# Optimization experiments

Measured on AMD Instinct MI355X. Metric: run time of the kernel, lower is better.

The kernel has to match this reference:

```python
import jax, jax.numpy as jnp
import numpy as np
import math

N_NODES = 100000
N_EDGES = 1600000
IN_CH = 128
EDGE_DIM = 8
HEADS = 4
C1, C2 = 10, 5  # per-head out channels of conv1/conv2
N_GRAPHS = 64


def setup_inputs() -> dict:
    key = jax.random.key(0)
    k = jax.random.split(key, 26)
    s = 0.05
    d1, d2 = HEADS * C1, HEADS * C2  # 40, 20
    lin = lambda kk, fi, fo: jax.random.normal(kk, (fi, fo), jnp.float32) * s
    inp = {}
    inp['x'] = jax.random.normal(k[0], (N_NODES, IN_CH), jnp.float32)
    inp['edge_index'] = jax.random.randint(k[1], (2, N_EDGES), 0, N_NODES)
    inp['edge_attr'] = jax.random.normal(k[2], (N_EDGES, EDGE_DIM), jnp.float32)
    inp['batch'] = jnp.sort(jax.random.randint(k[3], (N_NODES,), 0, N_GRAPHS))
    # conv1 params (TransformerConv: lin_query/key/value + lin_edge(no bias) + lin_skip)
    inp['Wq1'] = lin(k[4], IN_CH, d1); inp['bq1'] = jnp.zeros((d1,), jnp.float32)
    inp['Wk1'] = lin(k[5], IN_CH, d1); inp['bk1'] = jnp.zeros((d1,), jnp.float32)
    inp['Wv1'] = lin(k[6], IN_CH, d1); inp['bv1'] = jnp.zeros((d1,), jnp.float32)
    inp['We1'] = lin(k[7], EDGE_DIM, d1)
    inp['Ws1'] = lin(k[8], IN_CH, d1); inp['bs1'] = jnp.zeros((d1,), jnp.float32)
    # conv2 params
    inp['Wq2'] = lin(k[9], d1, d2); inp['bq2'] = jnp.zeros((d2,), jnp.float32)
    inp['Wk2'] = lin(k[10], d1, d2); inp['bk2'] = jnp.zeros((d2,), jnp.float32)
    inp['Wv2'] = lin(k[11], d1, d2); inp['bv2'] = jnp.zeros((d2,), jnp.float32)
    inp['We2'] = lin(k[12], EDGE_DIM, d2)
    inp['Ws2'] = lin(k[13], d1, d2); inp['bs2'] = jnp.zeros((d2,), jnp.float32)
    # MLP head
    inp['W1'] = lin(k[14], d2, 10); inp['b1'] = jnp.zeros((10,), jnp.float32)
    inp['W2'] = lin(k[15], 10, 3); inp['b2'] = jnp.zeros((3,), jnp.float32)
    return inp


def _segment_softmax(alpha, dst, n):
    # numerically stable softmax over incoming edges of each target node
    amax = jax.ops.segment_max(alpha, dst, num_segments=n)
    ex = jnp.exp(alpha - amax[dst])
    den = jax.ops.segment_sum(ex, dst, num_segments=n)
    return ex / (den[dst] + 1e-16)


def _transformer_conv(x, src, dst, eattr, Wq, bq, Wk, bk, Wv, bv, We, Ws, bs, heads, ch):
    n = x.shape[0]
    q = (x @ Wq + bq).reshape(n, heads, ch)
    k = (x @ Wk + bk).reshape(n, heads, ch)
    v = (x @ Wv + bv).reshape(n, heads, ch)
    e = (eattr @ We).reshape(-1, heads, ch)          # [E,H,C]
    kj = k[src] + e                                   # gather + edge bias
    alpha = jnp.einsum('ehc,ehc->eh', q[dst], kj) / math.sqrt(ch)
    alpha = _segment_softmax(alpha, dst, n)           # [E,H]
    msg = (v[src] + e) * alpha[:, :, None]
    out = jax.ops.segment_sum(msg, dst, num_segments=n).reshape(n, heads * ch)
    return out + x @ Ws + bs                          # root/skip connection (beta=False)


def reference(x, edge_index, edge_attr, batch, Wq1, bq1, Wk1, bk1, Wv1, bv1, We1, Ws1, bs1, Wq2, bq2, Wk2, bk2, Wv2, bv2, We2, Ws2, bs2, W1, b1, W2, b2):
    src, dst = edge_index[0], edge_index[1]
    h = jax.nn.relu(_transformer_conv(x, src, dst, edge_attr, Wq1, bq1, Wk1, bk1, Wv1, bv1, We1, Ws1, bs1, HEADS, C1))
    h = jax.nn.relu(_transformer_conv(h, src, dst, edge_attr, Wq2, bq2, Wk2, bk2, Wv2, bv2, We2, Ws2, bs2, HEADS, C2))
    # global_mean_pool
    sums = jax.ops.segment_sum(h, batch, num_segments=N_GRAPHS)
    cnt = jax.ops.segment_sum(jnp.ones((h.shape[0],), h.dtype), batch, num_segments=N_GRAPHS)
    pooled = sums / jnp.maximum(cnt, 1.0)[:, None]
    h = jax.nn.relu(pooled @ W1 + b1)
    return h @ W2 + b2
```

## Files before the change

kernel.cpp:

```cpp
#include <hip/hip_runtime.h>
#include <math.h>

__device__ __forceinline__ unsigned bfr_(float f) {
    unsigned u = __float_as_uint(f);
    return (u + 0x7fffu + ((u >> 16) & 1u)) >> 16;
}
__device__ __forceinline__ unsigned pack2_(float lo, float hi) {
    return bfr_(lo) | (bfr_(hi) << 16);
}
__device__ __forceinline__ float unlo_(unsigned u) { return __uint_as_float(u << 16); }
__device__ __forceinline__ float unhi_(unsigned u) { return __uint_as_float(u & 0xffff0000u); }
__device__ __forceinline__ float bf2f_(unsigned short us) {
    return __uint_as_float((unsigned)us << 16);
}

__global__ void k_hist(const int* __restrict__ dst, int* __restrict__ deg, int E) {
    int e = blockIdx.x * 256 + threadIdx.x;
    if (e < E) atomicAdd(&deg[dst[e]], 1);
}

__global__ void k_scan1(const int* __restrict__ deg, int* __restrict__ rp,
                        int* __restrict__ bsum, int n) {
    __shared__ int sh[256];
    int t = threadIdx.x;
    int base = blockIdx.x * 1024 + t * 4;
    int v0 = (base + 0 < n) ? deg[base + 0] : 0;
    int v1 = (base + 1 < n) ? deg[base + 1] : 0;
    int v2 = (base + 2 < n) ? deg[base + 2] : 0;
    int v3 = (base + 3 < n) ? deg[base + 3] : 0;
    int ts = v0 + v1 + v2 + v3;
    sh[t] = ts;
    __syncthreads();
    for (int off = 1; off < 256; off <<= 1) {
        int x = (t >= off) ? sh[t - off] : 0;
        __syncthreads();
        sh[t] += x;
        __syncthreads();
    }
    int run = sh[t] - ts;
    if (base + 0 < n) rp[base + 0] = run;
    run += v0;
    if (base + 1 < n) rp[base + 1] = run;
    run += v1;
    if (base + 2 < n) rp[base + 2] = run;
    run += v2;
    if (base + 3 < n) rp[base + 3] = run;
    if (t == 255) bsum[blockIdx.x] = sh[255];
}

__global__ void k_scan2(int* __restrict__ bsum, int nb) {
    __shared__ int sh[256];
    int t = threadIdx.x;
    int v = (t < nb) ? bsum[t] : 0;
    sh[t] = v;
    __syncthreads();
    for (int off = 1; off < 256; off <<= 1) {
        int x = (t >= off) ? sh[t - off] : 0;
        __syncthreads();
        sh[t] += x;
        __syncthreads();
    }
    if (t < nb) bsum[t] = sh[t] - v;
}

__global__ void k_scan3(int* __restrict__ rp, const int* __restrict__ bsum,
                        int* __restrict__ cur, int n, int total) {
    int t = threadIdx.x;
    int base = blockIdx.x * 1024 + t * 4;
    int add = bsum[blockIdx.x];
    if (base + 0 < n) { rp[base + 0] += add; cur[base + 0] = 0; }
    if (base + 1 < n) { rp[base + 1] += add; cur[base + 1] = 0; }
    if (base + 2 < n) { rp[base + 2] += add; cur[base + 2] = 0; }
    if (base + 3 < n) { rp[base + 3] += add; cur[base + 3] = 0; }
    if (blockIdx.x == 0 && t == 0) rp[n] = total;
}

__global__ void k_scatter(const int* __restrict__ src, const int* __restrict__ dst,
                          const int* __restrict__ rp, int* __restrict__ cur,
                          const float4* __restrict__ ea,
                          unsigned long long* __restrict__ se_perm,
                          uint4* __restrict__ eab, int E) {
    int e = blockIdx.x * 256 + threadIdx.x;
    if (e >= E) return;
    float4 a = ea[(size_t)e * 2 + 0];
    float4 b = ea[(size_t)e * 2 + 1];
    uint4 u;
    u.x = pack2_(a.x, a.y);
    u.y = pack2_(a.z, a.w);
    u.z = pack2_(b.x, b.y);
    u.w = pack2_(b.z, b.w);
    eab[e] = u;
    int d = dst[e];
    int pos = rp[d] + atomicAdd(&cur[d], 1);
    unsigned long long rec =
        ((unsigned long long)(unsigned)e << 32) | (unsigned)src[e];
    __builtin_nontemporal_store(rec, &se_perm[pos]);
}

template <int FIN, int CH, int KTILE, int NPT, int CHPAD>
__global__ __launch_bounds__(256) void k_proj(
    const float* __restrict__ X,
    const float* __restrict__ Wq, const float* __restrict__ Wk,
    const float* __restrict__ Wv, const float* __restrict__ Ws,
    const float* __restrict__ bq, const float* __restrict__ bk,
    const float* __restrict__ bv, const float* __restrict__ bs,
    float* __restrict__ qO, unsigned* __restrict__ kvO,
    unsigned short* __restrict__ sO, int N) {
    constexpr int FOUT = 4 * CH;
    constexpr int STRIDE = 4 * CHPAD;
    constexpr int NPB = 64;
    constexpr int COLS = 4 * FOUT;
    constexpr int NCG = COLS / 10;
    constexpr int NG = 256 / NCG;
    static_assert(NG * NPT == NPB, "geometry");
    constexpr int F4 = FIN / 4;
    __shared__ float xs[FIN * NPB];
    __shared__ float wbuf[KTILE * COLS];
    int t = threadIdx.x;
    int nb = blockIdx.x * NPB;
    for (int i = t; i < NPB * F4; i += 256) {
        int nl = i & 63;
        int k4 = (i >> 6) * 4;
        int node = nb + nl;
        float4 val = make_float4(0.f, 0.f, 0.f, 0.f);
        if (node < N) val = *(const float4*)(X + (size_t)node * FIN + k4);
        xs[(k4 + 0) * NPB + nl] = val.x;
        xs[(k4 + 1) * NPB + nl] = val.y;
        xs[(k4 + 2) * NPB + nl] = val.z;
        xs[(k4 + 3) * NPB + nl] = val.w;
    }
    int cg = t % NCG, ng = t / NCG;
    int which = (cg * 10) / FOUT, cc0 = (cg * 10) % FOUT;
    float acc[NPT][10];
#pragma unroll
    for (int i = 0; i < NPT; ++i)
#pragma unroll
        for (int j = 0; j < 10; ++j) acc[i][j] = 0.f;

    for (int kt = 0; kt < FIN; kt += KTILE) {
        __syncthreads();
        for (int i = t; i < KTILE * (COLS / 4); i += 256) {
            int kk = i / (COLS / 4);
            int c4 = (i % (COLS / 4)) * 4;
            int wh = c4 / FOUT, cc = c4 % FOUT;
            const float* Wsrc = wh == 0 ? Wq : wh == 1 ? Wk : wh == 2 ? Wv : Ws;
            float4 wv = *(const float4*)(Wsrc + (size_t)(kt + kk) * FOUT + cc);
            wbuf[kk * COLS + c4 + 0] = wv.x;
            wbuf[kk * COLS + c4 + 1] = wv.y;
            wbuf[kk * COLS + c4 + 2] = wv.z;
            wbuf[kk * COLS + c4 + 3] = wv.w;
        }
        __syncthreads();
#pragma unroll 4
        for (int kk = 0; kk < KTILE; ++kk) {
            float xv[NPT];
            if constexpr (NPT == 4) {
                float4 x4 = *(const float4*)(xs + (kt + kk) * NPB + ng * 4);
                xv[0] = x4.x; xv[1] = x4.y; xv[2] = x4.z; xv[3] = x4.w;
            } else {
                float2 x2 = *(const float2*)(xs + (kt + kk) * NPB + ng * 2);
                xv[0] = x2.x; xv[1] = x2.y;
            }
            const float2* wp = (const float2*)(wbuf + kk * COLS + cg * 10);
            float wv[10];
#pragma unroll
            for (int jj = 0; jj < 5; ++jj) {
                float2 w2 = wp[jj];
                wv[2 * jj] = w2.x;
                wv[2 * jj + 1] = w2.y;
            }
#pragma unroll
            for (int i = 0; i < NPT; ++i)
#pragma unroll
                for (int j = 0; j < 10; ++j) acc[i][j] += xv[i] * wv[j];
        }
    }
    const float* B = which == 0 ? bq : which == 1 ? bk : which == 2 ? bv : bs;
    float bias[10];
#pragma unroll
    for (int j = 0; j < 10; ++j) bias[j] = B[cc0 + j];
    __syncthreads();
    if (which == 0) {
#pragma unroll
        for (int i = 0; i < NPT; ++i) {
            int node = nb + ng * NPT + i;
            if (node < N)
#pragma unroll
                for (int j = 0; j < 10; ++j) {
                    int col = cc0 + j, hh = col / CH, cc = col % CH;
                    qO[(size_t)node * STRIDE + hh * CHPAD + cc] = acc[i][j] + bias[j];
                }
        }
    } else if (which == 3) {
#pragma unroll
        for (int i = 0; i < NPT; ++i) {
            int node = nb + ng * NPT + i;
            if (node < N)
#pragma unroll
                for (int j = 0; j < 10; ++j)
                    sO[(size_t)node * FOUT + cc0 + j] =
                        (unsigned short)bfr_(acc[i][j] + bias[j]);
        }
    } else if (which == 1) {
#pragma unroll
        for (int i = 0; i < NPT; ++i) {
            int nl = ng * NPT + i;
#pragma unroll
            for (int j = 0; j < 10; ++j) wbuf[nl * FOUT + cc0 + j] = acc[i][j] + bias[j];
        }
    }
    __syncthreads();
    if (which == 2) {
#pragma unroll
        for (int i = 0; i < NPT; ++i) {
            int nl = ng * NPT + i;
            int node = nb + nl;
            if (node < N)
#pragma unroll
                for (int j = 0; j < 10; ++j) {
                    int col = cc0 + j, hh = col / CH, cc = col % CH;
                    float kf = wbuf[nl * FOUT + cc0 + j];
                    kvO[(size_t)node * STRIDE + hh * CHPAD + cc] =
                        pack2_(kf, acc[i][j] + bias[j]);
                }
        }
    }
}

template <int CH, int CHPAD, bool SHIFT>
__global__ __launch_bounds__(256) void k_conv(
    const int* __restrict__ rp, const unsigned long long* __restrict__ se_perm,
    const uint4* __restrict__ eab, const float* __restrict__ We,
    const float* __restrict__ q, const unsigned* __restrict__ kv,
    const unsigned short* __restrict__ skp, float* __restrict__ hout,
    float inv_sqrt, int N) {
    constexpr int D = 4 * CH;
    constexpr int STRIDE = 4 * CHPAD;
    constexpr int RAWN = SHIFT ? CHPAD + 2 : CHPAD;
    constexpr int NLD = RAWN / 4;
    __shared__ float we_s[8 * D];
    for (int i = threadIdx.x; i < 8 * D; i += 256) we_s[i] = We[i];
    __syncthreads();
    int g = blockIdx.x * 256 + threadIdx.x;
    int node = g >> 4;
    int h = g & 3;
    int qtr = (g >> 2) & 3;
    if (node >= N) return;
    int start_off = SHIFT ? ((h * CH) & ~3) : h * CHPAD;
    int rs = rp[node], re = rp[node + 1];
    float qh[CH];
    {
        float qraw[RAWN];
        const float4* qp = (const float4*)(q + (size_t)node * STRIDE + start_off);
#pragma unroll
        for (int i = 0; i < NLD; ++i) *(float4*)&qraw[4 * i] = qp[i];
        if constexpr (SHIFT) {
            if (h & 1) {
#pragma unroll
                for (int c = 0; c < CH; ++c) qraw[c] = qraw[c + 2];
            }
        }
#pragma unroll
        for (int c = 0; c < CH; ++c) qh[c] = qraw[c];
    }
    float qe[8];
#pragma unroll
    for (int j = 0; j < 8; ++j) {
        float sE = 0.f;
#pragma unroll
        for (int c = 0; c < CH; ++c) sE += qh[c] * we_s[j * D + h * CH + c];
        qe[j] = sE;
    }
    float m = -3.0e38f, l = 0.f;
    float accv[CH] = {};
    float acce[8] = {};
    for (int p = rs + qtr; p < re; p += 4) {
        unsigned long long se = se_perm[p];
        int sidx = (int)(unsigned)(se & 0xffffffffu);
        int eid = (int)(unsigned)(se >> 32);
        uint4 eu = eab[eid];
        float ea8[8];
        ea8[0] = unlo_(eu.x); ea8[1] = unhi_(eu.x);
        ea8[2] = unlo_(eu.y); ea8[3] = unhi_(eu.y);
        ea8[4] = unlo_(eu.z); ea8[5] = unhi_(eu.z);
        ea8[6] = unlo_(eu.w); ea8[7] = unhi_(eu.w);
        unsigned kraw[RAWN];
        const uint4* kp = (const uint4*)(kv + (size_t)sidx * STRIDE + start_off);
#pragma unroll
        for (int i = 0; i < NLD; ++i) *(uint4*)&kraw[4 * i] = kp[i];
        if constexpr (SHIFT) {
            if (h & 1) {
#pragma unroll
                for (int c = 0; c < CH; ++c) kraw[c] = kraw[c + 2];
            }
        }
        float a = 0.f;
        float vj[CH];
#pragma unroll
        for (int c = 0; c < CH; ++c) {
            unsigned u = kraw[c];
            a += qh[c] * unlo_(u);
            vj[c] = unhi_(u);
        }
#pragma unroll
        for (int j = 0; j < 8; ++j) a += qe[j] * ea8[j];
        a *= inv_sqrt;
        float mn = fmaxf(m, a);
        float so = __expf(m - mn);
        float w = __expf(a - mn);
        l = l * so + w;
#pragma unroll
        for (int c = 0; c < CH; ++c) accv[c] = accv[c] * so + w * vj[c];
#pragma unroll
        for (int j = 0; j < 8; ++j) acce[j] = acce[j] * so + w * ea8[j];
        m = mn;
    }
#pragma unroll
    for (int mask = 4; mask <= 8; mask <<= 1) {
        float mo = __shfl_xor(m, mask);
        float lo = __shfl_xor(l, mask);
        float mn = fmaxf(m, mo);
        float s1 = (m > -1e37f) ? __expf(m - mn) : 0.f;
        float s2 = (mo > -1e37f) ? __expf(mo - mn) : 0.f;
        l = l * s1 + lo * s2;
#pragma unroll
        for (int c = 0; c < CH; ++c) {
            float ao = __shfl_xor(accv[c], mask);
            accv[c] = accv[c] * s1 + ao * s2;
        }
#pragma unroll
        for (int j = 0; j < 8; ++j) {
            float ao = __shfl_xor(acce[j], mask);
            acce[j] = acce[j] * s1 + ao * s2;
        }
        m = mn;
    }
    if (qtr == 0) {
        float inv = 1.0f / (l + 1e-16f);
#pragma unroll
        for (int c = 0; c < CH; ++c) {
            float ec = 0.f;
#pragma unroll
            for (int j = 0; j < 8; ++j) ec += acce[j] * we_s[j * D + h * CH + c];
            float o = (accv[c] + ec) * inv + bf2f_(skp[(size_t)node * D + h * CH + c]);
            hout[(size_t)node * D + h * CH + c] = fmaxf(o, 0.f);
        }
    }
}

__global__ void k_pool(const float* __restrict__ h2, const int* __restrict__ batch,
                       float* __restrict__ pooled, float* __restrict__ cnt, int N) {
    int t = blockIdx.x * 256 + threadIdx.x;
    int start = t * 16;
    if (start >= N) return;
    int end = min(start + 16, N);
    float acc[20];
#pragma unroll
    for (int c = 0; c < 20; ++c) acc[c] = 0.f;
    int cg = batch[start];
    float run = 0.f;
    for (int n = start; n < end; ++n) {
        int g = batch[n];
        if (g != cg) {
#pragma unroll
            for (int c = 0; c < 20; ++c) atomicAdd(&pooled[cg * 20 + c], acc[c]);
            atomicAdd(&cnt[cg], run);
#pragma unroll
            for (int c = 0; c < 20; ++c) acc[c] = 0.f;
            run = 0.f;
            cg = g;
        }
#pragma unroll
        for (int c = 0; c < 20; ++c) acc[c] += h2[(size_t)n * 20 + c];
        run += 1.f;
    }
#pragma unroll
    for (int c = 0; c < 20; ++c) atomicAdd(&pooled[cg * 20 + c], acc[c]);
    atomicAdd(&cnt[cg], run);
}

__global__ void k_mlp(const float* __restrict__ pooled, const float* __restrict__ cnt,
                      const float* __restrict__ W1, const float* __restrict__ b1,
                      const float* __restrict__ W2, const float* __restrict__ b2,
                      float* __restrict__ out) {
    int g = threadIdx.x;
    if (g >= 64) return;
    float ic = 1.0f / fmaxf(cnt[g], 1.0f);
    float p[20];
#pragma unroll
    for (int i = 0; i < 20; ++i) p[i] = pooled[g * 20 + i] * ic;
    float hid[10];
#pragma unroll
    for (int j = 0; j < 10; ++j) {
        float a = b1[j];
#pragma unroll
        for (int i = 0; i < 20; ++i) a += p[i] * W1[i * 10 + j];
        hid[j] = fmaxf(a, 0.f);
    }
#pragma unroll
    for (int o = 0; o < 3; ++o) {
        float a = b2[o];
#pragma unroll
        for (int j = 0; j < 10; ++j) a += hid[j] * W2[j * 3 + o];
        out[g * 3 + o] = a;
    }
}

extern "C" void kernel_launch(void* const* d_in, const int* in_sizes, int n_in,
                              void* d_out, int out_size, void* d_ws, size_t ws_size,
                              hipStream_t stream) {
    const float* x   = (const float*)d_in[0];
    const int* ei    = (const int*)d_in[1];
    const float* ea  = (const float*)d_in[2];
    const int* batch = (const int*)d_in[3];
    const float *Wq1 = (const float*)d_in[4],  *bq1 = (const float*)d_in[5];
    const float *Wk1 = (const float*)d_in[6],  *bk1 = (const float*)d_in[7];
    const float *Wv1 = (const float*)d_in[8],  *bv1 = (const float*)d_in[9];
    const float *We1 = (const float*)d_in[10];
    const float *Ws1 = (const float*)d_in[11], *bs1 = (const float*)d_in[12];
    const float *Wq2 = (const float*)d_in[13], *bq2 = (const float*)d_in[14];
    const float *Wk2 = (const float*)d_in[15], *bk2 = (const float*)d_in[16];
    const float *Wv2 = (const float*)d_in[17], *bv2 = (const float*)d_in[18];
    const float *We2 = (const float*)d_in[19];
    const float *Ws2 = (const float*)d_in[20], *bs2 = (const float*)d_in[21];
    const float *W1  = (const float*)d_in[22], *b1  = (const float*)d_in[23];
    const float *W2  = (const float*)d_in[24], *b2  = (const float*)d_in[25];

    const int N = in_sizes[0] / 128;
    const int E = in_sizes[1] / 2;
    const int* srcI = ei;
    const int* dstI = ei + E;

    float* F = (float*)d_ws;
    float*          q    = F;
    unsigned*       kv   = (unsigned*)(F + 4000000);
    float*          h1   = F + 8000000;
    float*          h2   = F + 8000000;
    unsigned short* s_bf = (unsigned short*)(F + 12000000);
    float*          pooled = F + 14000000;
    float*          cnt    = F + 14001280;
    int* I = (int*)(F + 14002048);
    int* deg  = I;
    int* cur  = I;
    int* rpR  = I + 100352;
    int* bsum = I + 200704;
    unsigned long long* se_perm = (unsigned long long*)(I + 200960);
    uint4* eab = (uint4*)(I + 200960 + 3200000);

    const int SCAN_BLOCKS = (N + 1023) / 1024;
    const int EB = (E + 255) / 256;

    hipMemsetAsync(deg, 0, (size_t)N * 4, stream);
    hipMemsetAsync(pooled, 0, (1280 + 64) * 4, stream);

    k_hist<<<EB, 256, 0, stream>>>(dstI, deg, E);
    k_scan1<<<SCAN_BLOCKS, 256, 0, stream>>>(deg, rpR, bsum, N);
    k_scan2<<<1, 256, 0, stream>>>(bsum, SCAN_BLOCKS);
    k_scan3<<<SCAN_BLOCKS, 256, 0, stream>>>(rpR, bsum, cur, N, E);
    k_scatter<<<EB, 256, 0, stream>>>(srcI, dstI, rpR, cur, (const float4*)ea,
                                      se_perm, eab, E);

    k_proj<128, 10, 32, 4, 10><<<(N + 63) / 64, 256, 0, stream>>>(
        x, Wq1, Wk1, Wv1, Ws1, bq1, bk1, bv1, bs1, q, kv, s_bf, N);
    k_conv<10, 10, true><<<(16 * N + 255) / 256, 256, 0, stream>>>(
        rpR, se_perm, eab, We1, q, kv, s_bf, h1, 0.31622776601683794f, N);

    k_proj<40, 5, 40, 2, 8><<<(N + 63) / 64, 256, 0, stream>>>(
        h1, Wq2, Wk2, Wv2, Ws2, bq2, bk2, bv2, bs2, q, kv, s_bf, N);
    k_conv<5, 8, false><<<(16 * N + 255) / 256, 256, 0, stream>>>(
        rpR, se_perm, eab, We2, q, kv, s_bf, h2, 0.4472135954999579f, N);

    k_pool<<<((N + 15) / 16 + 255) / 256, 256, 0, stream>>>(h2, batch, pooled, cnt, N);
    k_mlp<<<1, 64, 0, stream>>>(pooled, cnt, W1, b1, W2, b2, (float*)d_out);
}
```

Baseline: 578.7 us.

## Fuse edge packing into histogram and overlap scatter with first projection

Moves the bf16 packing of edge attributes out of the scatter kernel and into the histogram kernel, which now runs twice as many blocks with a block-index split. The CSR scatter is merged into the same launch as the first-layer projection, so the atomic-bound scatter blocks and the compute-bound GEMM blocks share the GPU. Projection blocks shrink to 32 nodes with smaller K tiles, and the second projection uses one node per thread. This removes a launch and tries to overlap latency-bound work, at the cost of lower per-block reuse in the projections and more shared memory sized for the scatter blocks, which do not use it.

```diff
diff --git a/kernel.cpp b/kernel.cpp
--- a/kernel.cpp
+++ b/kernel.cpp
@@ -14,9 +14,26 @@
     return __uint_as_float((unsigned)us << 16);
 }
 
-__global__ void k_hist(const int* __restrict__ dst, int* __restrict__ deg, int E) {
-    int e = blockIdx.x * 256 + threadIdx.x;
-    if (e < E) atomicAdd(&deg[dst[e]], 1);
+__global__ void k_hist_pack(const int* __restrict__ dstI, int* __restrict__ deg,
+                            const float4* __restrict__ ea, uint4* __restrict__ eab,
+                            int E, int HB) {
+    int bid = blockIdx.x;
+    if (bid < HB) {
+        int e = bid * 256 + threadIdx.x;
+        if (e < E) atomicAdd(&deg[dstI[e]], 1);
+    } else {
+        int e = (bid - HB) * 256 + threadIdx.x;
+        if (e < E) {
+            float4 a = ea[(size_t)e * 2 + 0];
+            float4 b = ea[(size_t)e * 2 + 1];
+            uint4 u;
+            u.x = pack2_(a.x, a.y);
+            u.y = pack2_(a.z, a.w);
+            u.z = pack2_(b.x, b.y);
+            u.w = pack2_(b.z, b.w);
+            eab[e] = u;
+        }
+    }
 }
 
 __global__ void k_scan1(const int* __restrict__ deg, int* __restrict__ rp,
@@ -75,52 +92,27 @@
     if (blockIdx.x == 0 && t == 0) rp[n] = total;
 }
 
-__global__ void k_scatter(const int* __restrict__ src, const int* __restrict__ dst,
-                          const int* __restrict__ rp, int* __restrict__ cur,
-                          const float4* __restrict__ ea,
-                          unsigned long long* __restrict__ se_perm,
-                          uint4* __restrict__ eab, int E) {
-    int e = blockIdx.x * 256 + threadIdx.x;
-    if (e >= E) return;
-    float4 a = ea[(size_t)e * 2 + 0];
-    float4 b = ea[(size_t)e * 2 + 1];
-    uint4 u;
-    u.x = pack2_(a.x, a.y);
-    u.y = pack2_(a.z, a.w);
-    u.z = pack2_(b.x, b.y);
-    u.w = pack2_(b.z, b.w);
-    eab[e] = u;
-    int d = dst[e];
-    int pos = rp[d] + atomicAdd(&cur[d], 1);
-    unsigned long long rec =
-        ((unsigned long long)(unsigned)e << 32) | (unsigned)src[e];
-    __builtin_nontemporal_store(rec, &se_perm[pos]);
-}
-
-template <int FIN, int CH, int KTILE, int NPT, int CHPAD>
-__global__ __launch_bounds__(256) void k_proj(
-    const float* __restrict__ X,
+template <int FIN, int CH, int KTILE, int NPT, int CHPAD, int NPB>
+__device__ __forceinline__ void proj_dev(
+    int pb, const float* __restrict__ X,
     const float* __restrict__ Wq, const float* __restrict__ Wk,
     const float* __restrict__ Wv, const float* __restrict__ Ws,
     const float* __restrict__ bq, const float* __restrict__ bk,
     const float* __restrict__ bv, const float* __restrict__ bs,
     float* __restrict__ qO, unsigned* __restrict__ kvO,
-    unsigned short* __restrict__ sO, int N) {
+    unsigned short* __restrict__ sO, int N, float* xs, float* wbuf) {
     constexpr int FOUT = 4 * CH;
     constexpr int STRIDE = 4 * CHPAD;
-    constexpr int NPB = 64;
     constexpr int COLS = 4 * FOUT;
     constexpr int NCG = COLS / 10;
     constexpr int NG = 256 / NCG;
     static_assert(NG * NPT == NPB, "geometry");
     constexpr int F4 = FIN / 4;
-    __shared__ float xs[FIN * NPB];
-    __shared__ float wbuf[KTILE * COLS];
     int t = threadIdx.x;
-    int nb = blockIdx.x * NPB;
+    int nb = pb * NPB;
     for (int i = t; i < NPB * F4; i += 256) {
-        int nl = i & 63;
-        int k4 = (i >> 6) * 4;
+        int nl = i % NPB;
+        int k4 = (i / NPB) * 4;
         int node = nb + nl;
         float4 val = make_float4(0.f, 0.f, 0.f, 0.f);
         if (node < N) val = *(const float4*)(X + (size_t)node * FIN + k4);
@@ -157,9 +149,11 @@
             if constexpr (NPT == 4) {
                 float4 x4 = *(const float4*)(xs + (kt + kk) * NPB + ng * 4);
                 xv[0] = x4.x; xv[1] = x4.y; xv[2] = x4.z; xv[3] = x4.w;
-            } else {
+            } else if constexpr (NPT == 2) {
                 float2 x2 = *(const float2*)(xs + (kt + kk) * NPB + ng * 2);
                 xv[0] = x2.x; xv[1] = x2.y;
+            } else {
+                xv[0] = xs[(kt + kk) * NPB + ng];
             }
             const float2* wp = (const float2*)(wbuf + kk * COLS + cg * 10);
             float wv[10];
@@ -225,6 +219,50 @@
                 }
         }
     }
+}
+
+template <int FIN, int CH, int KTILE, int NPT, int CHPAD, int NPB>
+__global__ __launch_bounds__(256) void k_proj(
+    const float* __restrict__ X,
+    const float* __restrict__ Wq, const float* __restrict__ Wk,
+    const float* __restrict__ Wv, const float* __restrict__ Ws,
+    const float* __restrict__ bq, const float* __restrict__ bk,
+    const float* __restrict__ bv, const float* __restrict__ bs,
+    float* __restrict__ qO, unsigned* __restrict__ kvO,
+    unsigned short* __restrict__ sO, int N) {
+    __shared__ float xs[FIN * NPB];
+    __shared__ float wbuf[KTILE * 16 * CH];
+    proj_dev<FIN, CH, KTILE, NPT, CHPAD, NPB>(blockIdx.x, X, Wq, Wk, Wv, Ws, bq, bk,
+                                              bv, bs, qO, kvO, sO, N, xs, wbuf);
+}
+
+template <int FIN, int CH, int KTILE, int NPT, int CHPAD, int NPB>
+__global__ __launch_bounds__(256) void k_scatter_proj(
+    const int* __restrict__ srcI, const int* __restrict__ dstI,
+    const int* __restrict__ rp, int* __restrict__ cur,
+    unsigned long long* __restrict__ se_perm, int E, int SB,
+    const float* __restrict__ X,
+    const float* __restrict__ Wq, const float* __restrict__ Wk,
+    const float* __restrict__ Wv, const float* __restrict__ Ws,
+    const float* __restrict__ bq, const float* __restrict__ bk,
+    const float* __restrict__ bv, const float* __restrict__ bs,
+    float* __restrict__ qO, unsigned* __restrict__ kvO,
+    unsigned short* __restrict__ sO, int N) {
+    __shared__ float xs[FIN * NPB];
+    __shared__ float wbuf[KTILE * 16 * CH];
+    if (blockIdx.x < SB) {
+        int e = blockIdx.x * 256 + threadIdx.x;
+        if (e < E) {
+            int d = dstI[e];
+            int pos = rp[d] + atomicAdd(&cur[d], 1);
+            unsigned long long rec =
+                ((unsigned long long)(unsigned)e << 32) | (unsigned)srcI[e];
+            __builtin_nontemporal_store(rec, &se_perm[pos]);
+        }
+        return;
+    }
+    proj_dev<FIN, CH, KTILE, NPT, CHPAD, NPB>(blockIdx.x - SB, X, Wq, Wk, Wv, Ws, bq,
+                                              bk, bv, bs, qO, kvO, sO, N, xs, wbuf);
 }
 
 template <int CH, int CHPAD, bool SHIFT>
@@ -449,23 +487,23 @@
 
     const int SCAN_BLOCKS = (N + 1023) / 1024;
     const int EB = (E + 255) / 256;
+    const int PB = (N + 31) / 32;
 
     hipMemsetAsync(deg, 0, (size_t)N * 4, stream);
     hipMemsetAsync(pooled, 0, (1280 + 64) * 4, stream);
 
-    k_hist<<<EB, 256, 0, stream>>>(dstI, deg, E);
+    k_hist_pack<<<2 * EB, 256, 0, stream>>>(dstI, deg, (const float4*)ea, eab, E, EB);
     k_scan1<<<SCAN_BLOCKS, 256, 0, stream>>>(deg, rpR, bsum, N);
     k_scan2<<<1, 256, 0, stream>>>(bsum, SCAN_BLOCKS);
     k_scan3<<<SCAN_BLOCKS, 256, 0, stream>>>(rpR, bsum, cur, N, E);
-    k_scatter<<<EB, 256, 0, stream>>>(srcI, dstI, rpR, cur, (const float4*)ea,
-                                      se_perm, eab, E);
-
-    k_proj<128, 10, 32, 4, 10><<<(N + 63) / 64, 256, 0, stream>>>(
+
+    k_scatter_proj<128, 10, 16, 2, 10, 32><<<EB + PB, 256, 0, stream>>>(
+        srcI, dstI, rpR, cur, se_perm, E, EB,
         x, Wq1, Wk1, Wv1, Ws1, bq1, bk1, bv1, bs1, q, kv, s_bf, N);
     k_conv<10, 10, true><<<(16 * N + 255) / 256, 256, 0, stream>>>(
         rpR, se_perm, eab, We1, q, kv, s_bf, h1, 0.31622776601683794f, N);
 
-    k_proj<40, 5, 40, 2, 8><<<(N + 63) / 64, 256, 0, stream>>>(
+    k_proj<40, 5, 40, 1, 8, 32><<<PB, 256, 0, stream>>>(
         h1, Wq2, Wk2, Wv2, Ws2, bq2, bk2, bv2, bs2, q, kv, s_bf, N);
     k_conv<5, 8, false><<<(16 * N + 255) / 256, 256, 0, stream>>>(
         rpR, se_perm, eab, We2, q, kv, s_bf, h2, 0.4472135954999579f, N);
```

Result: slower. 607.6 us (+5.0%).

## Store edge attributes in CSR order and shrink proj tiles for conv2

Applied to the files above, without the earlier changes.

The scatter kernel now writes the bf16-packed edge attributes and the source index directly at the CSR position, instead of storing a packed (edge id, src) record plus edge attributes indexed by original edge id. This removes the dependent random gather of edge attributes in both conv kernels, turning it into a sequential read along the CSR row. Separately, conv1's projection uses a smaller K tile (8), and conv2's projection uses 32 nodes per block with one node per thread. That gives more blocks and less shared memory per block, at the cost of less register reuse. The scatter now performs random-position 16-byte writes, and the workspace layout is reshuffled to fit the larger permuted edge array.

```diff
diff --git a/kernel.cpp b/kernel.cpp
--- a/kernel.cpp
+++ b/kernel.cpp
@@ -77,9 +77,8 @@
 
 __global__ void k_scatter(const int* __restrict__ src, const int* __restrict__ dst,
                           const int* __restrict__ rp, int* __restrict__ cur,
-                          const float4* __restrict__ ea,
-                          unsigned long long* __restrict__ se_perm,
-                          uint4* __restrict__ eab, int E) {
+                          const float4* __restrict__ ea, int* __restrict__ src_perm,
+                          uint4* __restrict__ eap, int E) {
     int e = blockIdx.x * 256 + threadIdx.x;
     if (e >= E) return;
     float4 a = ea[(size_t)e * 2 + 0];
@@ -89,15 +88,13 @@
     u.y = pack2_(a.z, a.w);
     u.z = pack2_(b.x, b.y);
     u.w = pack2_(b.z, b.w);
-    eab[e] = u;
     int d = dst[e];
     int pos = rp[d] + atomicAdd(&cur[d], 1);
-    unsigned long long rec =
-        ((unsigned long long)(unsigned)e << 32) | (unsigned)src[e];
-    __builtin_nontemporal_store(rec, &se_perm[pos]);
-}
-
-template <int FIN, int CH, int KTILE, int NPT, int CHPAD>
+    src_perm[pos] = src[e];
+    eap[pos] = u;
+}
+
+template <int FIN, int CH, int KTILE, int NPT, int CHPAD, int NPB>
 __global__ __launch_bounds__(256) void k_proj(
     const float* __restrict__ X,
     const float* __restrict__ Wq, const float* __restrict__ Wk,
@@ -108,7 +105,6 @@
     unsigned short* __restrict__ sO, int N) {
     constexpr int FOUT = 4 * CH;
     constexpr int STRIDE = 4 * CHPAD;
-    constexpr int NPB = 64;
     constexpr int COLS = 4 * FOUT;
     constexpr int NCG = COLS / 10;
     constexpr int NG = 256 / NCG;
@@ -119,8 +115,8 @@
     int t = threadIdx.x;
     int nb = blockIdx.x * NPB;
     for (int i = t; i < NPB * F4; i += 256) {
-        int nl = i & 63;
-        int k4 = (i >> 6) * 4;
+        int nl = i % NPB;
+        int k4 = (i / NPB) * 4;
         int node = nb + nl;
         float4 val = make_float4(0.f, 0.f, 0.f, 0.f);
         if (node < N) val = *(const float4*)(X + (size_t)node * FIN + k4);
@@ -157,9 +153,11 @@
             if constexpr (NPT == 4) {
                 float4 x4 = *(const float4*)(xs + (kt + kk) * NPB + ng * 4);
                 xv[0] = x4.x; xv[1] = x4.y; xv[2] = x4.z; xv[3] = x4.w;
-            } else {
+            } else if constexpr (NPT == 2) {
                 float2 x2 = *(const float2*)(xs + (kt + kk) * NPB + ng * 2);
                 xv[0] = x2.x; xv[1] = x2.y;
+            } else {
+                xv[0] = xs[(kt + kk) * NPB + ng];
             }
             const float2* wp = (const float2*)(wbuf + kk * COLS + cg * 10);
             float wv[10];
@@ -229,8 +227,8 @@
 
 template <int CH, int CHPAD, bool SHIFT>
 __global__ __launch_bounds__(256) void k_conv(
-    const int* __restrict__ rp, const unsigned long long* __restrict__ se_perm,
-    const uint4* __restrict__ eab, const float* __restrict__ We,
+    const int* __restrict__ rp, const int* __restrict__ src_perm,
+    const uint4* __restrict__ eap, const float* __restrict__ We,
     const float* __restrict__ q, const unsigned* __restrict__ kv,
     const unsigned short* __restrict__ skp, float* __restrict__ hout,
     float inv_sqrt, int N) {
@@ -275,10 +273,8 @@
     float accv[CH] = {};
     float acce[8] = {};
     for (int p = rs + qtr; p < re; p += 4) {
-        unsigned long long se = se_perm[p];
-        int sidx = (int)(unsigned)(se & 0xffffffffu);
-        int eid = (int)(unsigned)(se >> 32);
-        uint4 eu = eab[eid];
+        int sidx = src_perm[p];
+        uint4 eu = eap[p];
         float ea8[8];
         ea8[0] = unlo_(eu.x); ea8[1] = unhi_(eu.x);
         ea8[2] = unlo_(eu.y); ea8[3] = unhi_(eu.y);
@@ -437,15 +433,15 @@
     float*          h1   = F + 8000000;
     float*          h2   = F + 8000000;
     unsigned short* s_bf = (unsigned short*)(F + 12000000);
-    float*          pooled = F + 14000000;
-    float*          cnt    = F + 14001280;
-    int* I = (int*)(F + 14002048);
+    uint4*          eap  = (uint4*)(F + 14000000);
+    int*       src_perm  = (int*)(F + 20400000);
+    int* I = (int*)(F + 22000000);
     int* deg  = I;
     int* cur  = I;
     int* rpR  = I + 100352;
     int* bsum = I + 200704;
-    unsigned long long* se_perm = (unsigned long long*)(I + 200960);
-    uint4* eab = (uint4*)(I + 200960 + 3200000);
+    float* pooled = F + 22300000;
+    float* cnt    = pooled + 1280;
 
     const int SCAN_BLOCKS = (N + 1023) / 1024;
     const int EB = (E + 255) / 256;
@@ -458,17 +454,17 @@
     k_scan2<<<1, 256, 0, stream>>>(bsum, SCAN_BLOCKS);
     k_scan3<<<SCAN_BLOCKS, 256, 0, stream>>>(rpR, bsum, cur, N, E);
     k_scatter<<<EB, 256, 0, stream>>>(srcI, dstI, rpR, cur, (const float4*)ea,
-                                      se_perm, eab, E);
-
-    k_proj<128, 10, 32, 4, 10><<<(N + 63) / 64, 256, 0, stream>>>(
+                                      src_perm, eap, E);
+
+    k_proj<128, 10, 8, 4, 10, 64><<<(N + 63) / 64, 256, 0, stream>>>(
         x, Wq1, Wk1, Wv1, Ws1, bq1, bk1, bv1, bs1, q, kv, s_bf, N);
     k_conv<10, 10, true><<<(16 * N + 255) / 256, 256, 0, stream>>>(
-        rpR, se_perm, eab, We1, q, kv, s_bf, h1, 0.31622776601683794f, N);
-
-    k_proj<40, 5, 40, 2, 8><<<(N + 63) / 64, 256, 0, stream>>>(
+        rpR, src_perm, eap, We1, q, kv, s_bf, h1, 0.31622776601683794f, N);
+
+    k_proj<40, 5, 40, 1, 8, 32><<<(N + 31) / 32, 256, 0, stream>>>(
         h1, Wq2, Wk2, Wv2, Ws2, bq2, bk2, bv2, bs2, q, kv, s_bf, N);
     k_conv<5, 8, false><<<(16 * N + 255) / 256, 256, 0, stream>>>(
-        rpR, se_perm, eab, We2, q, kv, s_bf, h2, 0.4472135954999579f, N);
+        rpR, src_perm, eap, We2, q, kv, s_bf, h2, 0.4472135954999579f, N);
 
     k_pool<<<((N + 15) / 16 + 255) / 256, 256, 0, stream>>>(h2, batch, pooled, cnt, N);
     k_mlp<<<1, 64, 0, stream>>>(pooled, cnt, W1, b1, W2, b2, (float*)d_out);
```

Measured after the change: 524.1 us. 9.4% less time.
